# Performance work log

Measured on AMD Instinct MI355X. Metric: run time of the kernel, lower is better.

The kernel has to match this reference:

```python
import jax, jax.numpy as jnp
import numpy as np

KERNEL = (3, 3, 3, 3)
PAD = (1, 1, 1, 1)
IN_CH = 8
OUT_CH = 8


def setup_inputs() -> dict:
    key = jax.random.key(0)
    k1, k2, k3 = jax.random.split(key, 3)
    x = jax.random.normal(k1, (2, IN_CH, 7, 7, 48, 48), dtype=jnp.float32)
    K = KERNEL[0] * KERNEL[1] * KERNEL[2] * KERNEL[3]
    conv = jax.random.normal(k2, (OUT_CH, K * IN_CH), dtype=jnp.float32) * 0.05
    bias = jax.random.normal(k3, (OUT_CH,), dtype=jnp.float32) * 0.05
    return {"x": x, "conv": conv, "bias": bias}


def reference(x, conv, bias):
    # x: (B, C, u, v, h, w); conv: (oc, k0*k1*k2*k3*C); bias: (oc,)
    B, C, u, v, h, w = x.shape
    oc = conv.shape[0]
    k0, k1, k2, k3 = KERNEL
    # torch unfold+permute orders the contraction axis as (k0,k1,k2,k3,C)
    W = conv.reshape(oc, k0, k1, k2, k3, C)
    xp = jnp.pad(x, ((0, 0), (0, 0),
                     (PAD[0], PAD[0]), (PAD[1], PAD[1]),
                     (PAD[2], PAD[2]), (PAD[3], PAD[3])))
    out = jnp.zeros((B, oc, u, v, h, w), dtype=x.dtype)
    # stride = 1 everywhere: accumulate over the 3^4 kernel offsets
    for i0 in range(k0):
        for i1 in range(k1):
            for i2 in range(k2):
                for i3 in range(k3):
                    xs = xp[:, :, i0:i0 + u, i1:i1 + v, i2:i2 + h, i3:i3 + w]
                    out = out + jnp.einsum('bcuvhw,oc->bouvhw', xs,
                                           W[:, i0, i1, i2, i3, :])
    out = out + bias[None, :, None, None, None, None]
    return out
```

## Files before the change

### kernel.cpp

```cpp
#include <hip/hip_runtime.h>


typedef __attribute__((ext_vector_type(8))) short short8;
typedef __attribute__((ext_vector_type(4))) float f32x4;

#define CSTRIDE (49 * 2304)
#define ZS_OFF  3920000
#define WP_OFF  3960000
#define WT_OFF  3987648

__device__ __forceinline__ unsigned short f2bf(float f) {
    union { float f; unsigned u; } v; v.f = f;
    unsigned u = v.u;
    return (unsigned short)((u + 0x7FFF + ((u >> 16) & 1)) >> 16);
}

__global__ __launch_bounds__(256)
void prep(const float* __restrict__ x, const float* __restrict__ conv,
          unsigned short* __restrict__ ws16) {
    int g = blockIdx.x * 256 + threadIdx.x;
    if (g < 247500) {
        unsigned short vals[8];
#pragma unroll
        for (int c = 0; c < 8; ++c) vals[c] = 0;
        if (g < 245000) {
            int b  = g / 122500;
            int r  = g - b * 122500;
            int uv = r / 2500;
            int p  = r - uv * 2500;
            int hh = p / 50, ww = p - hh * 50;
            int h = hh - 1, w = ww - 1;
            if (((unsigned)h < 48u) && ((unsigned)w < 48u)) {
                const float* xb = x + ((size_t)b * 8 * 49 + uv) * 2304 + h * 48 + w;
#pragma unroll
                for (int c = 0; c < 8; ++c) vals[c] = f2bf(xb[(size_t)c * CSTRIDE]);
            }
        }
        *(short8*)(ws16 + (size_t)g * 8) = *(const short8*)vals;
        return;
    }
    g -= 247500;
    if (g < 13824) {
        int as   = g >> 9;
        int r    = g & 511;
        int lane = r >> 3, j = r & 7;
        int m = lane & 15, q = lane >> 4;
        int o = m & 7, d = m >> 3;
        int i0i1 = as / 3, i3 = as - 3 * i0i1;
        int i2 = q - d;
        unsigned short v = 0;
        if ((unsigned)i2 < 3u)
            v = f2bf(conv[o * 648 + ((i0i1 * 3 + i2) * 3 + i3) * 8 + j]);
        ws16[WP_OFF / 2 + g] = v;
        return;
    }
    g -= 13824;
    if (g < 882) {
        int img = g / 9, k = g - img * 9;
        int b   = img / 49, uv = img - b * 49;
        int u   = uv / 7,   v  = uv - u * 7;
        int entry = ZS_OFF;
        int cnt = 0;
        for (int i01 = 0; i01 < 9; ++i01) {
            int i0 = i01 / 3, i1 = i01 - 3 * i0;
            int uu = u + i0 - 1, vv = v + i1 - 1;
            if (((unsigned)uu < 7u) && ((unsigned)vv < 7u)) {
                if (cnt == k)
                    entry = (((b * 7 + uu) * 7 + vv) * 40000) | (i01 << 22);
                ++cnt;
            }
        }
        ((int*)((char*)ws16 + WT_OFF))[g] = entry;
    }
}

__global__ __launch_bounds__(128, 4)
void conv4d_mfma(const unsigned short* __restrict__ ws16,
                 const float* __restrict__ bias,
                 float* __restrict__ out) {
    const int img = blockIdx.y;
    const int b   = img / 49;
    const int uvr = img - b * 49;
    const int u   = uvr / 7;
    const int v   = uvr - u * 7;
    const int cu  = 3 - (u == 0) - (u == 6);
    const int cv  = 3 - (v == 0) - (v == 6);
    const int nchunk = cu * cv * 3;

    const int lane = threadIdx.x & 63;
    const int wave = threadIdx.x >> 6;
    const int n    = lane & 15;
    const int quad = lane >> 4;

    const int widx = blockIdx.x * 2 + wave;
    const int dt0  = widx * 2;
    const int rp0  = dt0 / 3,        w00 = (dt0 - 3 * rp0) * 16;
    const int dt1  = dt0 + 1;
    const int rp1  = dt1 / 3,        w01 = (dt1 - 3 * rp1) * 16;

    const int myoff0 = ((rp0 * 2 + quad) * 50 + w00 + n) * 16;
    const int myoff1 = ((rp1 * 2 + quad) * 50 + w01 + n) * 16;

    const char* base0  = (const char*)ws16;
    const char* wpb    = base0 + WP_OFF;
    const int   lane16 = lane * 16;

    const int* tblp = (const int*)(base0 + WT_OFF) + img * 9;
    int t[9];
#pragma unroll
    for (int k = 0; k < 9; ++k) t[k] = tblp[k];

    f32x4 acc0 = (f32x4){0.f, 0.f, 0.f, 0.f};
    f32x4 acc1 = acc0;

#define CHUNK(c)                                                               \
    {                                                                          \
        int sl = (c) / 3, i3 = (c) % 3;                                        \
        int e   = t[sl];                                                       \
        int tab = (e & 0x3FFFFF) + i3 * 16;                                    \
        int wof = (((e >> 22) * 3 + i3) << 10);                                \
        short8 wf  = *(const short8*)(wpb + wof + lane16);                     \
        const char* xb = base0 + tab;                                          \
        short8 xf0 = *(const short8*)(xb + myoff0);                            \
        short8 xf1 = *(const short8*)(xb + myoff1);                            \
        acc0 = __builtin_amdgcn_mfma_f32_16x16x32_bf16(wf, xf0, acc0, 0, 0, 0);\
        acc1 = __builtin_amdgcn_mfma_f32_16x16x32_bf16(wf, xf1, acc1, 0, 0, 0);\
    }

#pragma unroll
    for (int c = 0; c < 12; ++c) CHUNK(c);
    if (nchunk > 12) {
#pragma unroll
        for (int c = 12; c < 18; ++c) CHUNK(c);
        if (nchunk > 18) {
#pragma unroll
            for (int c = 18; c < 27; ++c) CHUNK(c);
        }
    }
#undef CHUNK

    {
        const int d  = quad >> 1;
        const int oq = (quad & 1) * 4;
        const f32x4 bb = *(const f32x4*)(bias + oq);
        float* obase = out + ((size_t)(b * 8 + oq) * 49 + uvr) * 2304;
        float* ob0 = obase + (rp0 * 2 + d) * 48 + w00 + n;
        float* ob1 = obase + (rp1 * 2 + d) * 48 + w01 + n;
#pragma unroll
        for (int r = 0; r < 4; ++r) {
            ob0[(size_t)r * CSTRIDE] = acc0[r] + bb[r];
            ob1[(size_t)r * CSTRIDE] = acc1[r] + bb[r];
        }
    }
}

extern "C" void kernel_launch(void* const* d_in, const int* in_sizes, int n_in,
                              void* d_out, int out_size, void* d_ws, size_t ws_size,
                              hipStream_t stream) {
    const float* x    = (const float*)d_in[0];
    const float* conv = (const float*)d_in[1];
    const float* bias = (const float*)d_in[2];
    float* out = (float*)d_out;
    unsigned short* ws16 = (unsigned short*)d_ws;

    prep<<<dim3((247500 + 13824 + 882 + 255) / 256), dim3(256), 0, stream>>>(x, conv, ws16);
    conv4d_mfma<<<dim3(18, 98), dim3(128), 0, stream>>>(ws16, bias, out);
}
```

Baseline: 74.75 us.

## Split 4D conv reduction across two blocks with atomic accumulation into bias-initialized output

Adds a grid z-dimension of 2 so each image's (i0,i1) kernel slices are divided between two blocks, which roughly halves the serial MFMA chain per block and doubles the number of blocks in flight. The prep kernel now also fills the output with bias, and the conv kernel accumulates its partial sums with float atomics instead of plain stores. The launch-bounds occupancy hint is raised from 4 to 7. The cost is double the output traffic, atomic read-modify-write latency, an extra output-initialization pass, and summation order that is no longer deterministic.

```diff
diff --git a/kernel.cpp b/kernel.cpp
--- a/kernel.cpp
+++ b/kernel.cpp
@@ -17,7 +17,8 @@
 
 __global__ __launch_bounds__(256)
 void prep(const float* __restrict__ x, const float* __restrict__ conv,
-          unsigned short* __restrict__ ws16) {
+          const float* __restrict__ bias,
+          unsigned short* __restrict__ ws16, float* __restrict__ out) {
     int g = blockIdx.x * 256 + threadIdx.x;
     if (g < 247500) {
         unsigned short vals[8];
@@ -71,21 +72,30 @@
             }
         }
         ((int*)((char*)ws16 + WT_OFF))[g] = entry;
+        return;
+    }
+    g -= 882;
+    if (g < 451584) {
+        int plane = g / 28224;
+        float bv = bias[plane & 7];
+        f32x4 val = (f32x4){bv, bv, bv, bv};
+        ((f32x4*)out)[g] = val;
     }
 }
 
-__global__ __launch_bounds__(128, 4)
+__global__ __launch_bounds__(128, 7)
 void conv4d_mfma(const unsigned short* __restrict__ ws16,
-                 const float* __restrict__ bias,
                  float* __restrict__ out) {
     const int img = blockIdx.y;
+    const int par = blockIdx.z;
     const int b   = img / 49;
     const int uvr = img - b * 49;
     const int u   = uvr / 7;
     const int v   = uvr - u * 7;
     const int cu  = 3 - (u == 0) - (u == 6);
     const int cv  = 3 - (v == 0) - (v == 6);
-    const int nchunk = cu * cv * 3;
+    const int nv  = cu * cv;
+    const int count = (nv + 1 - par) >> 1;
 
     const int lane = threadIdx.x & 63;
     const int wave = threadIdx.x >> 6;
@@ -106,50 +116,53 @@
     const int   lane16 = lane * 16;
 
     const int* tblp = (const int*)(base0 + WT_OFF) + img * 9;
-    int t[9];
+    int t[5];
 #pragma unroll
-    for (int k = 0; k < 9; ++k) t[k] = tblp[k];
+    for (int i = 0; i < 5; ++i) {
+        int idx = par + 2 * i;
+        t[i] = tblp[idx > 8 ? 8 : idx];
+    }
 
     f32x4 acc0 = (f32x4){0.f, 0.f, 0.f, 0.f};
     f32x4 acc1 = acc0;
 
-#define CHUNK(c)                                                               \
+#define SLICE(i)                                                               \
     {                                                                          \
-        int sl = (c) / 3, i3 = (c) % 3;                                        \
-        int e   = t[sl];                                                       \
-        int tab = (e & 0x3FFFFF) + i3 * 16;                                    \
-        int wof = (((e >> 22) * 3 + i3) << 10);                                \
-        short8 wf  = *(const short8*)(wpb + wof + lane16);                     \
-        const char* xb = base0 + tab;                                          \
-        short8 xf0 = *(const short8*)(xb + myoff0);                            \
-        short8 xf1 = *(const short8*)(xb + myoff1);                            \
-        acc0 = __builtin_amdgcn_mfma_f32_16x16x32_bf16(wf, xf0, acc0, 0, 0, 0);\
-        acc1 = __builtin_amdgcn_mfma_f32_16x16x32_bf16(wf, xf1, acc1, 0, 0, 0);\
+        int e = t[i];                                                          \
+        _Pragma("unroll")                                                      \
+        for (int i3 = 0; i3 < 3; ++i3) {                                       \
+            int tab = (e & 0x3FFFFF) + i3 * 16;                                \
+            int wof = (((e >> 22) * 3 + i3) << 10);                            \
+            short8 wf  = *(const short8*)(wpb + wof + lane16);                 \
+            const char* xb = base0 + tab;                                      \
+            short8 xf0 = *(const short8*)(xb + myoff0);                        \
+            short8 xf1 = *(const short8*)(xb + myoff1);                        \
+            acc0 = __builtin_amdgcn_mfma_f32_16x16x32_bf16(wf, xf0, acc0, 0, 0, 0); \
+            acc1 = __builtin_amdgcn_mfma_f32_16x16x32_bf16(wf, xf1, acc1, 0, 0, 0); \
+        }                                                                      \
     }
 
-#pragma unroll
-    for (int c = 0; c < 12; ++c) CHUNK(c);
-    if (nchunk > 12) {
-#pragma unroll
-        for (int c = 12; c < 18; ++c) CHUNK(c);
-        if (nchunk > 18) {
-#pragma unroll
-            for (int c = 18; c < 27; ++c) CHUNK(c);
+    SLICE(0);
+    SLICE(1);
+    if (count > 2) {
+        SLICE(2);
+        if (count > 3) {
+            SLICE(3);
+            if (count > 4) SLICE(4);
         }
     }
-#undef CHUNK
+#undef SLICE
 
     {
         const int d  = quad >> 1;
         const int oq = (quad & 1) * 4;
-        const f32x4 bb = *(const f32x4*)(bias + oq);
         float* obase = out + ((size_t)(b * 8 + oq) * 49 + uvr) * 2304;
         float* ob0 = obase + (rp0 * 2 + d) * 48 + w00 + n;
         float* ob1 = obase + (rp1 * 2 + d) * 48 + w01 + n;
 #pragma unroll
         for (int r = 0; r < 4; ++r) {
-            ob0[(size_t)r * CSTRIDE] = acc0[r] + bb[r];
-            ob1[(size_t)r * CSTRIDE] = acc1[r] + bb[r];
+            unsafeAtomicAdd(&ob0[(size_t)r * CSTRIDE], acc0[r]);
+            unsafeAtomicAdd(&ob1[(size_t)r * CSTRIDE], acc1[r]);
         }
     }
 }
@@ -163,6 +176,8 @@
     float* out = (float*)d_out;
     unsigned short* ws16 = (unsigned short*)d_ws;
 
-    prep<<<dim3((247500 + 13824 + 882 + 255) / 256), dim3(256), 0, stream>>>(x, conv, ws16);
-    conv4d_mfma<<<dim3(18, 98), dim3(128), 0, stream>>>(ws16, bias, out);
+    int prep_threads = 247500 + 13824 + 882 + 451584;
+    prep<<<dim3((prep_threads + 255) / 256), dim3(256), 0, stream>>>(
+        x, conv, bias, ws16, out);
+    conv4d_mfma<<<dim3(18, 98, 2), dim3(128), 0, stream>>>(ws16, out);
 }
```

Measured after the change: 81.85 us. +9.5%, slower.
